# Optimization experiments

Measured on AMD Instinct MI355X. Metric: run time of the kernel, lower is better.

The kernel has to match this reference:

```python
import jax, jax.numpy as jnp
import numpy as np

# dims: StyleGAN2 modulated conv at 64x64, 512 channels
B, IC, OC, K, SD, H, W = 16, 512, 512, 3, 512, 64, 64
EPS = 1e-8


def setup_inputs() -> dict:
    key = jax.random.key(0)
    k1, k2, k3, k4 = jax.random.split(key, 4)
    return {
        "input": jax.random.normal(k1, (B, IC, H, W), dtype=jnp.float32),
        "style": jax.random.normal(k2, (B, SD), dtype=jnp.float32),
        # learned params
        "weight": jax.random.normal(k3, (1, OC, IC, K, K), dtype=jnp.float32),
        "mod_weight": jax.random.normal(k4, (IC, SD), dtype=jnp.float32),
        "mod_bias": jnp.ones((IC,), dtype=jnp.float32),  # bias_init=1
    }


def reference(input, style, weight, mod_weight, mod_bias):
    conv_scale = 1.0 / np.sqrt(IC * K * K)   # 1/sqrt(fan_in)
    mod_scale = 1.0 / np.sqrt(SD)            # EqualLinear scale, lr_mul=1

    # style modulation: EqualLinear(style_dim -> in_channel), no activation
    s = style @ (mod_weight * mod_scale).T + mod_bias          # [B, IC]

    # per-sample modulated weight [B, OC, IC, K, K]
    w = conv_scale * weight * s[:, None, :, None, None]
    # demodulation over (in_channel, kh, kw)
    demod = jax.lax.rsqrt(jnp.sum(w * w, axis=(2, 3, 4)) + EPS)  # [B, OC]
    w = w * demod[:, :, None, None, None]

    # grouped conv with groups=batch (same trick as torch F.conv2d groups=B)
    x = input.reshape(1, B * IC, H, W)
    wg = w.reshape(B * OC, IC, K, K)
    pad = K // 2
    out = jax.lax.conv_general_dilated(
        x, wg,
        window_strides=(1, 1),
        padding=[(pad, pad), (pad, pad)],
        dimension_numbers=("NCHW", "OIHW", "NCHW"),
        feature_group_count=B,
    )
    return out.reshape(B, OC, H, W)
```

## Files before the change

### kernel.cpp

```cpp
#include <hip/hip_runtime.h>
#include <hip/hip_bf16.h>

constexpr int BB = 16, IC = 512, OC = 512, HH = 64, WW = 64, HW = 64 * 64, SD = 512;
constexpr float MOD_SCALE = 0.04419417382415922f;
constexpr float CONV_SCALE = 0.014731391274719739f;
constexpr float CONV_SCALE2 = 2.170138888888889e-4f;

typedef float f32x4 __attribute__((ext_vector_type(4)));
typedef short bf16x8 __attribute__((ext_vector_type(8)));

__device__ __forceinline__ unsigned short f2bf(float x) {
  __hip_bfloat16 h = __float2bfloat16(x);
  return *(unsigned short*)&h;
}

__global__ void k_style(const float* __restrict__ style, const float* __restrict__ mw,
                        const float* __restrict__ mb, float* __restrict__ s) {
  __shared__ float st[SD];
  const int b = blockIdx.x;
  for (int i = threadIdx.x; i < SD; i += 256) st[i] = style[b * SD + i];
  __syncthreads();
  for (int ic = threadIdx.x; ic < IC; ic += 256) {
    const float4* wr = (const float4*)(mw + (size_t)ic * SD);
    float acc = 0.f;
    for (int d = 0; d < SD / 4; ++d) {
      float4 w4 = wr[d];
      float4 s4 = *(const float4*)&st[d * 4];
      acc += w4.x * s4.x + w4.y * s4.y + w4.z * s4.z + w4.w * s4.w;
    }
    s[b * IC + ic] = acc * MOD_SCALE + mb[ic];
  }
}

__global__ void k_pack(const float* __restrict__ w, unsigned short* __restrict__ wpack,
                       float* __restrict__ w2sum) {
  const int oc = blockIdx.x;
  const int ic0 = threadIdx.x * 2;
  const float* p = w + (size_t)oc * IC * 9 + (size_t)ic0 * 9;
  float v[18];
#pragma unroll
  for (int i = 0; i < 18; ++i) v[i] = p[i];
  float s0 = 0.f, s1 = 0.f;
#pragma unroll
  for (int t = 0; t < 9; ++t) { s0 += v[t] * v[t]; s1 += v[9 + t] * v[9 + t]; }
  *(float2*)&w2sum[oc * IC + ic0] = make_float2(s0, s1);
#pragma unroll
  for (int t = 0; t < 9; ++t) {
    unsigned int pk = (unsigned int)f2bf(v[t]) | ((unsigned int)f2bf(v[9 + t]) << 16);
    *(unsigned int*)&wpack[((size_t)t * OC + oc) * IC + ic0] = pk;
  }
}

__global__ void k_demod(const float* __restrict__ s, const float* __restrict__ w2sum,
                        float* __restrict__ fscale) {
  __shared__ float s2[IC];
  const int b = blockIdx.x;
  for (int i = threadIdx.x; i < IC; i += 256) { float v = s[b * IC + i]; s2[i] = v * v; }
  __syncthreads();
  for (int oc = threadIdx.x; oc < OC; oc += 256) {
    const float4* wr = (const float4*)(w2sum + (size_t)oc * IC);
    float acc = 0.f;
    for (int i4 = 0; i4 < IC / 4; ++i4) {
      float4 w4 = wr[i4];
      float4 q4 = *(const float4*)&s2[i4 * 4];
      acc += w4.x * q4.x + w4.y * q4.y + w4.z * q4.z + w4.w * q4.w;
    }
    fscale[b * OC + oc] = CONV_SCALE * rsqrtf(CONV_SCALE2 * acc + 1e-8f);
  }
}

__global__ __launch_bounds__(256) void k_conv(
    const float* __restrict__ x, const unsigned short* __restrict__ wpack,
    const float* __restrict__ s, const float* __restrict__ fscale,
    float* __restrict__ out) {
  __shared__ __align__(128) unsigned short Asm[3][128 * 32];
  __shared__ __align__(128) unsigned short Bsm[264 * 32];

  const int bx = blockIdx.x;
  const int b = bx >> 7;
  const int mblk = (bx >> 5) & 3;
  const int nblk = bx & 31;

  const int tid = threadIdx.x;
  const int wave = tid >> 6, lane = tid & 63;
  const int wm = wave >> 1, wn = wave & 1;
  const int lrow = lane & 15, lk = lane >> 4;

  const int h0 = nblk * 2;
  const float* xb = x + (size_t)b * IC * HW;
  const float* sb = s + b * IC;

  f32x4 acc[4][4];
#pragma unroll
  for (int i = 0; i < 4; ++i)
#pragma unroll
    for (int j = 0; j < 4; ++j) acc[i][j] = f32x4{0.f, 0.f, 0.f, 0.f};

  {
    int q = tid >> 5;
    int hh = q >> 1, wz = (q & 1) ? 65 : 0;
    Bsm[(hh * 66 + wz) * 32 + (tid & 31)] = 0;
  }

  auto stageB = [&](int icb) {
    const int hh = wave;
    const int w = lane;
    const int h_abs = h0 - 1 + hh;
    const bool vh = (h_abs >= 0) && (h_abs < HH);
    const int h_safe = vh ? h_abs : 0;
    const int r = hh * 66 + w + 1;
    const int swz = (r >> 1) & 3;
    const float* src = xb + (size_t)(icb * 32) * HW + h_safe * WW + w;
#pragma unroll
    for (int c = 0; c < 4; ++c) {
      unsigned int pk[4];
#pragma unroll
      for (int jj = 0; jj < 4; ++jj) {
        int ic = c * 8 + jj * 2;
        float m0 = vh ? sb[icb * 32 + ic] : 0.f;
        float m1 = vh ? sb[icb * 32 + ic + 1] : 0.f;
        float v0 = src[(size_t)ic * HW] * m0;
        float v1 = src[(size_t)(ic + 1) * HW] * m1;
        pk[jj] = (unsigned int)f2bf(v0) | ((unsigned int)f2bf(v1) << 16);
      }
      int cd = c ^ swz;
      *(uint4*)&Bsm[r * 32 + cd * 8] = make_uint4(pk[0], pk[1], pk[2], pk[3]);
    }
  };

  auto issueA = [&](int tap, int icb, int nb) {
    const unsigned short* base =
        wpack + ((size_t)(tap * OC + mblk * 128)) * IC + icb * 32;
#pragma unroll
    for (int q = 0; q < 2; ++q) {
      int r = wave * 32 + q * 16 + (lane >> 2);
      int c = lane & 3;
      int cs = c ^ ((r >> 1) & 3);
      const unsigned short* g = base + (size_t)r * IC + cs * 8;
      unsigned short* l = &Asm[nb][(wave * 32 + q * 16) * 32];
      __builtin_amdgcn_global_load_lds(
          (const __attribute__((address_space(1))) void*)g,
          (__attribute__((address_space(3))) void*)l, 16, 0, 0);
    }
  };

  stageB(0);
  issueA(0, 0, 0);
  issueA(1, 0, 1);
  __syncthreads();

  for (int icb = 0; icb < 16; ++icb) {
#pragma unroll
    for (int t = 0; t < 9; ++t) {
      if (t == 8) {
        if (icb == 15) asm volatile("s_waitcnt vmcnt(0)" ::: "memory");
        else           asm volatile("s_waitcnt vmcnt(2)" ::: "memory");
      } else {
        asm volatile("s_waitcnt vmcnt(2)" ::: "memory");
      }
      __builtin_amdgcn_s_barrier();
      __builtin_amdgcn_sched_barrier(0);

      if (t == 0 && icb > 0) {
        stageB(icb);
        asm volatile("s_waitcnt lgkmcnt(0)" ::: "memory");
        __builtin_amdgcn_s_barrier();
        __builtin_amdgcn_sched_barrier(0);
      }

      if (t <= 6) {
        issueA(t + 2, icb, (t + 2) % 3);
      } else if (icb < 15) {
        issueA(t - 7, icb + 1, t - 7);
      }

      bf16x8 af[4], bfr[4];
#pragma unroll
      for (int i = 0; i < 4; ++i) {
        int r = wm * 64 + i * 16 + lrow;
        af[i] = *(const bf16x8*)&Asm[t % 3][r * 32 + ((lk ^ ((r >> 1) & 3)) * 8)];
      }
      const int dh = t / 3 - 1, dw = t % 3 - 1;
      const int hb = wn + dh + 1;
#pragma unroll
      for (int j = 0; j < 4; ++j) {
        int r = hb * 66 + j * 16 + lrow + dw + 1;
        bfr[j] = *(const bf16x8*)&Bsm[r * 32 + ((lk ^ ((r >> 1) & 3)) * 8)];
      }
      __builtin_amdgcn_s_setprio(1);
#pragma unroll
      for (int i = 0; i < 4; ++i)
#pragma unroll
        for (int j = 0; j < 4; ++j)
          acc[i][j] =
              __builtin_amdgcn_mfma_f32_16x16x32_bf16(af[i], bfr[j], acc[i][j], 0, 0, 0);
      __builtin_amdgcn_s_setprio(0);
      __builtin_amdgcn_sched_barrier(0);
    }
  }

  const float* fsb = fscale + b * OC;
#pragma unroll
  for (int i = 0; i < 4; ++i) {
#pragma unroll
    for (int rr = 0; rr < 4; ++rr) {
      const int oc = mblk * 128 + wm * 64 + i * 16 + lk * 4 + rr;
      const float sc = fsb[oc];
      float* orow = out + ((size_t)(b * OC + oc)) * HW + nblk * 128 + wn * 64 + lrow;
#pragma unroll
      for (int j = 0; j < 4; ++j) orow[j * 16] = acc[i][j][rr] * sc;
    }
  }
}

extern "C" void kernel_launch(void* const* d_in, const int* in_sizes, int n_in,
                              void* d_out, int out_size, void* d_ws, size_t ws_size,
                              hipStream_t stream) {
  const float* input = (const float*)d_in[0];
  const float* style = (const float*)d_in[1];
  const float* weight = (const float*)d_in[2];
  const float* mod_weight = (const float*)d_in[3];
  const float* mod_bias = (const float*)d_in[4];
  float* out = (float*)d_out;

  char* ws = (char*)d_ws;
  constexpr size_t WPACK_B = (size_t)9 * OC * IC * 2;
  constexpr size_t W2SUM_B = (size_t)OC * IC * 4;
  constexpr size_t S_B = (size_t)BB * IC * 4;
  unsigned short* wpack = (unsigned short*)ws;
  float* w2sum = (float*)(ws + WPACK_B);
  float* s = (float*)(ws + WPACK_B + W2SUM_B);
  float* fscale = (float*)(ws + WPACK_B + W2SUM_B + S_B);

  k_style<<<BB, 256, 0, stream>>>(style, mod_weight, mod_bias, s);
  k_pack<<<OC, 256, 0, stream>>>(weight, wpack, w2sum);
  k_demod<<<BB, 256, 0, stream>>>(s, w2sum, fscale);
  k_conv<<<2048, 256, 0, stream>>>(input, wpack, s, fscale, out);
}
```

Baseline: 474.3 us.

## Deepen A-tile ring, drop per-tap barriers, prefetch input into registers

The A weight tiles now use a 4-deep LDS ring loaded three taps ahead. Each wave loads and reads only its own 32 rows, so the per-tap block-wide barriers are removed and only vmcnt waits remain. The next input-channel block of x is loaded into registers in the middle of the tap loop and written to LDS between blocks, which hides the global load latency of the B staging. The wave tiling changes from a 2x2 layout to a 4x1 layout (32 OC by 128 pixels per wave), and launch bounds request 3 blocks per CU. The cost is more registers for xv and more LDS, plus hand-tuned waitcnt counts that must match the exact load ordering.

```diff
diff --git a/kernel.cpp b/kernel.cpp
--- a/kernel.cpp
+++ b/kernel.cpp
@@ -8,6 +8,8 @@
 
 typedef float f32x4 __attribute__((ext_vector_type(4)));
 typedef short bf16x8 __attribute__((ext_vector_type(8)));
+
+#define VMWAIT(n) asm volatile("s_waitcnt vmcnt(" #n ")" ::: "memory")
 
 __device__ __forceinline__ unsigned short f2bf(float x) {
   __hip_bfloat16 h = __float2bfloat16(x);
@@ -69,32 +71,27 @@
   }
 }
 
-__global__ __launch_bounds__(256) void k_conv(
+__global__ __launch_bounds__(256, 3) void k_conv(
     const float* __restrict__ x, const unsigned short* __restrict__ wpack,
     const float* __restrict__ s, const float* __restrict__ fscale,
     float* __restrict__ out) {
-  __shared__ __align__(128) unsigned short Asm[3][128 * 32];
+  __shared__ __align__(128) unsigned short Asm[4][128 * 32];
   __shared__ __align__(128) unsigned short Bsm[264 * 32];
 
   const int bx = blockIdx.x;
-  const int b = bx >> 7;
-  const int mblk = (bx >> 5) & 3;
-  const int nblk = bx & 31;
-
+  const int b = bx >> 7, mblk = (bx >> 5) & 3, nblk = bx & 31;
   const int tid = threadIdx.x;
   const int wave = tid >> 6, lane = tid & 63;
-  const int wm = wave >> 1, wn = wave & 1;
   const int lrow = lane & 15, lk = lane >> 4;
-
   const int h0 = nblk * 2;
   const float* xb = x + (size_t)b * IC * HW;
   const float* sb = s + b * IC;
 
-  f32x4 acc[4][4];
-#pragma unroll
-  for (int i = 0; i < 4; ++i)
-#pragma unroll
-    for (int j = 0; j < 4; ++j) acc[i][j] = f32x4{0.f, 0.f, 0.f, 0.f};
+  f32x4 acc[2][8];
+#pragma unroll
+  for (int i = 0; i < 2; ++i)
+#pragma unroll
+    for (int j = 0; j < 8; ++j) acc[i][j] = f32x4{0.f, 0.f, 0.f, 0.f};
 
   {
     int q = tid >> 5;
@@ -102,40 +99,39 @@
     Bsm[(hh * 66 + wz) * 32 + (tid & 31)] = 0;
   }
 
-  auto stageB = [&](int icb) {
-    const int hh = wave;
-    const int w = lane;
-    const int h_abs = h0 - 1 + hh;
-    const bool vh = (h_abs >= 0) && (h_abs < HH);
-    const int h_safe = vh ? h_abs : 0;
-    const int r = hh * 66 + w + 1;
-    const int swz = (r >> 1) & 3;
-    const float* src = xb + (size_t)(icb * 32) * HW + h_safe * WW + w;
+  const int sh = h0 - 1 + wave;
+  const bool vh = (sh >= 0) && (sh < HH);
+  const int shs = vh ? sh : 0;
+  const int brow = wave * 66 + lane + 1;
+  const int bswz = (brow >> 1) & 3;
+
+  float xv[32];
+  auto ld_x = [&](int icb) {
+    const float* src = xb + (size_t)(icb * 32) * HW + shs * WW + lane;
+#pragma unroll
+    for (int k = 0; k < 32; ++k) xv[k] = src[(size_t)k * HW];
+  };
+  auto wr_B = [&](int icb) {
 #pragma unroll
     for (int c = 0; c < 4; ++c) {
       unsigned int pk[4];
 #pragma unroll
       for (int jj = 0; jj < 4; ++jj) {
-        int ic = c * 8 + jj * 2;
-        float m0 = vh ? sb[icb * 32 + ic] : 0.f;
-        float m1 = vh ? sb[icb * 32 + ic + 1] : 0.f;
-        float v0 = src[(size_t)ic * HW] * m0;
-        float v1 = src[(size_t)(ic + 1) * HW] * m1;
-        pk[jj] = (unsigned int)f2bf(v0) | ((unsigned int)f2bf(v1) << 16);
+        int k = c * 8 + jj * 2;
+        float m0 = vh ? sb[icb * 32 + k] : 0.f;
+        float m1 = vh ? sb[icb * 32 + k + 1] : 0.f;
+        pk[jj] = (unsigned int)f2bf(xv[k] * m0) | ((unsigned int)f2bf(xv[k + 1] * m1) << 16);
       }
-      int cd = c ^ swz;
-      *(uint4*)&Bsm[r * 32 + cd * 8] = make_uint4(pk[0], pk[1], pk[2], pk[3]);
-    }
-  };
-
+      *(uint4*)&Bsm[brow * 32 + ((c ^ bswz) * 8)] = make_uint4(pk[0], pk[1], pk[2], pk[3]);
+    }
+  };
   auto issueA = [&](int tap, int icb, int nb) {
     const unsigned short* base =
         wpack + ((size_t)(tap * OC + mblk * 128)) * IC + icb * 32;
 #pragma unroll
     for (int q = 0; q < 2; ++q) {
       int r = wave * 32 + q * 16 + (lane >> 2);
-      int c = lane & 3;
-      int cs = c ^ ((r >> 1) & 3);
+      int cs = (lane & 3) ^ ((r >> 1) & 3);
       const unsigned short* g = base + (size_t)r * IC + cs * 8;
       unsigned short* l = &Asm[nb][(wave * 32 + q * 16) * 32];
       __builtin_amdgcn_global_load_lds(
@@ -144,71 +140,83 @@
     }
   };
 
-  stageB(0);
+  auto do_tap = [&](int t, int bufr) {
+    bf16x8 af[2], bfr[8];
+#pragma unroll
+    for (int i = 0; i < 2; ++i) {
+      int r = wave * 32 + i * 16 + lrow;
+      af[i] = *(const bf16x8*)&Asm[bufr][r * 32 + ((lk ^ ((r >> 1) & 3)) * 8)];
+    }
+    const int dh = t / 3 - 1, dw = t % 3 - 1;
+#pragma unroll
+    for (int j = 0; j < 8; ++j) {
+      int r = ((j >> 2) + dh + 1) * 66 + (j & 3) * 16 + lrow + dw + 1;
+      bfr[j] = *(const bf16x8*)&Bsm[r * 32 + ((lk ^ ((r >> 1) & 3)) * 8)];
+    }
+    __builtin_amdgcn_s_setprio(1);
+#pragma unroll
+    for (int i = 0; i < 2; ++i)
+#pragma unroll
+      for (int j = 0; j < 8; ++j)
+        acc[i][j] =
+            __builtin_amdgcn_mfma_f32_16x16x32_bf16(af[i], bfr[j], acc[i][j], 0, 0, 0);
+    __builtin_amdgcn_s_setprio(0);
+  };
+
+  ld_x(0);
   issueA(0, 0, 0);
   issueA(1, 0, 1);
-  __syncthreads();
-
-  for (int icb = 0; icb < 16; ++icb) {
+  issueA(2, 0, 2);
+  wr_B(0);
+  asm volatile("s_waitcnt lgkmcnt(0)" ::: "memory");
+  __builtin_amdgcn_sched_barrier(0);
+  __builtin_amdgcn_s_barrier();
+
+  int pb = 0;
+  for (int icb = 0; icb < 15; ++icb) {
 #pragma unroll
     for (int t = 0; t < 9; ++t) {
-      if (t == 8) {
-        if (icb == 15) asm volatile("s_waitcnt vmcnt(0)" ::: "memory");
-        else           asm volatile("s_waitcnt vmcnt(2)" ::: "memory");
-      } else {
-        asm volatile("s_waitcnt vmcnt(2)" ::: "memory");
+      if (t < 6) VMWAIT(4); else VMWAIT(20);
+      if (t + 3 <= 8) issueA(t + 3, icb, (pb + t + 3) & 3);
+      else            issueA(t - 6, icb + 1, (pb + t + 3) & 3);
+      if (t == 5) ld_x(icb + 1);
+      do_tap(t, (pb + t) & 3);
+    }
+    __builtin_amdgcn_s_barrier();
+    __builtin_amdgcn_sched_barrier(0);
+    wr_B(icb + 1);
+    asm volatile("s_waitcnt lgkmcnt(0)" ::: "memory");
+    __builtin_amdgcn_sched_barrier(0);
+    __builtin_amdgcn_s_barrier();
+    pb += 9;
+  }
+#pragma unroll
+  for (int t = 0; t < 9; ++t) {
+    if (t < 6) {
+      VMWAIT(4);
+      issueA(t + 3, 15, (pb + t + 3) & 3);
+    } else if (t == 6) {
+      VMWAIT(4);
+    } else if (t == 7) {
+      VMWAIT(2);
+    } else {
+      VMWAIT(0);
+    }
+    do_tap(t, (pb + t) & 3);
+  }
+
+  const float* fsb = fscale + b * OC;
+#pragma unroll
+  for (int i = 0; i < 2; ++i) {
+#pragma unroll
+    for (int rr = 0; rr < 4; ++rr) {
+      const int oc = mblk * 128 + wave * 32 + i * 16 + lk * 4 + rr;
+      const float sc = fsb[oc];
+#pragma unroll
+      for (int j = 0; j < 8; ++j) {
+        out[((size_t)(b * OC + oc)) * HW + (h0 + (j >> 2)) * WW + (j & 3) * 16 + lrow] =
+            acc[i][j][rr] * sc;
       }
-      __builtin_amdgcn_s_barrier();
-      __builtin_amdgcn_sched_barrier(0);
-
-      if (t == 0 && icb > 0) {
-        stageB(icb);
-        asm volatile("s_waitcnt lgkmcnt(0)" ::: "memory");
-        __builtin_amdgcn_s_barrier();
-        __builtin_amdgcn_sched_barrier(0);
-      }
-
-      if (t <= 6) {
-        issueA(t + 2, icb, (t + 2) % 3);
-      } else if (icb < 15) {
-        issueA(t - 7, icb + 1, t - 7);
-      }
-
-      bf16x8 af[4], bfr[4];
-#pragma unroll
-      for (int i = 0; i < 4; ++i) {
-        int r = wm * 64 + i * 16 + lrow;
-        af[i] = *(const bf16x8*)&Asm[t % 3][r * 32 + ((lk ^ ((r >> 1) & 3)) * 8)];
-      }
-      const int dh = t / 3 - 1, dw = t % 3 - 1;
-      const int hb = wn + dh + 1;
-#pragma unroll
-      for (int j = 0; j < 4; ++j) {
-        int r = hb * 66 + j * 16 + lrow + dw + 1;
-        bfr[j] = *(const bf16x8*)&Bsm[r * 32 + ((lk ^ ((r >> 1) & 3)) * 8)];
-      }
-      __builtin_amdgcn_s_setprio(1);
-#pragma unroll
-      for (int i = 0; i < 4; ++i)
-#pragma unroll
-        for (int j = 0; j < 4; ++j)
-          acc[i][j] =
-              __builtin_amdgcn_mfma_f32_16x16x32_bf16(af[i], bfr[j], acc[i][j], 0, 0, 0);
-      __builtin_amdgcn_s_setprio(0);
-      __builtin_amdgcn_sched_barrier(0);
-    }
-  }
-
-  const float* fsb = fscale + b * OC;
-#pragma unroll
-  for (int i = 0; i < 4; ++i) {
-#pragma unroll
-    for (int rr = 0; rr < 4; ++rr) {
-      const int oc = mblk * 128 + wm * 64 + i * 16 + lk * 4 + rr;
-      const float sc = fsb[oc];
-      float* orow = out + ((size_t)(b * OC + oc)) * HW + nblk * 128 + wn * 64 + lrow;
-#pragma unroll
-      for (int j = 0; j < 4; ++j) orow[j * 16] = acc[i][j][rr] * sc;
     }
   }
 }
```

Measured after the change: 658.4 us. +38.8%, slower.

## Deepen A-tile prefetch to four LDS buffers and double-buffer B fragments

Applied to the files above, without the earlier changes.

Grows the weight-tile LDS ring from three to four buffers so async global-to-LDS loads run three taps ahead, relaxing the vmcnt waits. B fragments for the next tap are read from LDS between MFMA groups into a second register buffer, overlapping LDS reads with matrix math. Launch bounds now request three blocks per SIMD/CU, which caps registers and may force spills given the larger fragment state and extra LDS per block.

```diff
diff --git a/kernel.cpp b/kernel.cpp
--- a/kernel.cpp
+++ b/kernel.cpp
@@ -8,6 +8,8 @@
 
 typedef float f32x4 __attribute__((ext_vector_type(4)));
 typedef short bf16x8 __attribute__((ext_vector_type(8)));
+
+#define VMWAIT(n) asm volatile("s_waitcnt vmcnt(" #n ")" ::: "memory")
 
 __device__ __forceinline__ unsigned short f2bf(float x) {
   __hip_bfloat16 h = __float2bfloat16(x);
@@ -69,11 +71,11 @@
   }
 }
 
-__global__ __launch_bounds__(256) void k_conv(
+__global__ __launch_bounds__(256, 3) void k_conv(
     const float* __restrict__ x, const unsigned short* __restrict__ wpack,
     const float* __restrict__ s, const float* __restrict__ fscale,
     float* __restrict__ out) {
-  __shared__ __align__(128) unsigned short Asm[3][128 * 32];
+  __shared__ __align__(128) unsigned short Asm[4][128 * 32];
   __shared__ __align__(128) unsigned short Bsm[264 * 32];
 
   const int bx = blockIdx.x;
@@ -134,8 +136,7 @@
 #pragma unroll
     for (int q = 0; q < 2; ++q) {
       int r = wave * 32 + q * 16 + (lane >> 2);
-      int c = lane & 3;
-      int cs = c ^ ((r >> 1) & 3);
+      int cs = (lane & 3) ^ ((r >> 1) & 3);
       const unsigned short* g = base + (size_t)r * IC + cs * 8;
       unsigned short* l = &Asm[nb][(wave * 32 + q * 16) * 32];
       __builtin_amdgcn_global_load_lds(
@@ -144,56 +145,65 @@
     }
   };
 
+  auto loadB = [&](bf16x8* dst, int tn) {
+    const int dh = tn / 3 - 1, dw = tn % 3 - 1;
+    const int hb = wn + dh + 1;
+#pragma unroll
+    for (int j = 0; j < 4; ++j) {
+      int r = hb * 66 + j * 16 + lrow + dw + 1;
+      dst[j] = *(const bf16x8*)&Bsm[r * 32 + ((lk ^ ((r >> 1) & 3)) * 8)];
+    }
+  };
+
   stageB(0);
   issueA(0, 0, 0);
   issueA(1, 0, 1);
+  issueA(2, 0, 2);
   __syncthreads();
 
+  bf16x8 bfr[2][4];
+
   for (int icb = 0; icb < 16; ++icb) {
 #pragma unroll
     for (int t = 0; t < 9; ++t) {
-      if (t == 8) {
-        if (icb == 15) asm volatile("s_waitcnt vmcnt(0)" ::: "memory");
-        else           asm volatile("s_waitcnt vmcnt(2)" ::: "memory");
-      } else {
-        asm volatile("s_waitcnt vmcnt(2)" ::: "memory");
-      }
+      if (icb == 15 && t == 7)      { VMWAIT(2); }
+      else if (icb == 15 && t == 8) { VMWAIT(0); }
+      else                          { VMWAIT(4); }
       __builtin_amdgcn_s_barrier();
       __builtin_amdgcn_sched_barrier(0);
 
-      if (t == 0 && icb > 0) {
-        stageB(icb);
-        asm volatile("s_waitcnt lgkmcnt(0)" ::: "memory");
-        __builtin_amdgcn_s_barrier();
-        __builtin_amdgcn_sched_barrier(0);
+      if (t == 0) {
+        if (icb > 0) {
+          stageB(icb);
+          asm volatile("s_waitcnt lgkmcnt(0)" ::: "memory");
+          __builtin_amdgcn_s_barrier();
+          __builtin_amdgcn_sched_barrier(0);
+        }
+        loadB(bfr[0], 0);
       }
 
-      if (t <= 6) {
-        issueA(t + 2, icb, (t + 2) % 3);
-      } else if (icb < 15) {
-        issueA(t - 7, icb + 1, t - 7);
-      }
-
-      bf16x8 af[4], bfr[4];
+      if (t <= 5)          issueA(t + 3, icb, (icb + t + 3) & 3);
+      else if (icb < 15)   issueA(t - 6, icb + 1, (icb + t + 3) & 3);
+
+      bf16x8 af[4];
 #pragma unroll
       for (int i = 0; i < 4; ++i) {
         int r = wm * 64 + i * 16 + lrow;
-        af[i] = *(const bf16x8*)&Asm[t % 3][r * 32 + ((lk ^ ((r >> 1) & 3)) * 8)];
+        af[i] = *(const bf16x8*)&Asm[(icb + t) & 3][r * 32 + ((lk ^ ((r >> 1) & 3)) * 8)];
       }
-      const int dh = t / 3 - 1, dw = t % 3 - 1;
-      const int hb = wn + dh + 1;
-#pragma unroll
-      for (int j = 0; j < 4; ++j) {
-        int r = hb * 66 + j * 16 + lrow + dw + 1;
-        bfr[j] = *(const bf16x8*)&Bsm[r * 32 + ((lk ^ ((r >> 1) & 3)) * 8)];
-      }
+
       __builtin_amdgcn_s_setprio(1);
 #pragma unroll
-      for (int i = 0; i < 4; ++i)
+      for (int j = 0; j < 4; ++j)
+        acc[0][j] = __builtin_amdgcn_mfma_f32_16x16x32_bf16(af[0], bfr[t & 1][j],
+                                                            acc[0][j], 0, 0, 0);
+      if (t < 8) loadB(bfr[(t + 1) & 1], t + 1);
+#pragma unroll
+      for (int i = 1; i < 4; ++i)
 #pragma unroll
         for (int j = 0; j < 4; ++j)
-          acc[i][j] =
-              __builtin_amdgcn_mfma_f32_16x16x32_bf16(af[i], bfr[j], acc[i][j], 0, 0, 0);
+          acc[i][j] = __builtin_amdgcn_mfma_f32_16x16x32_bf16(af[i], bfr[t & 1][j],
+                                                              acc[i][j], 0, 0, 0);
       __builtin_amdgcn_s_setprio(0);
       __builtin_amdgcn_sched_barrier(0);
     }
```

After: 892.9 us. 88.3% more time.

## Give each wave private weight rows to drop per-tap barriers

Applied to the files above, without the earlier changes.

The wave tiling changes from 2x2 (64x64 per wave) to 4x1 (32 output channels x 128 pixels per wave). Each wave now reads only the weight-tile rows it loaded itself through global_load_lds, so the block-wide barrier before every tap can be dropped. Only the per-channel-block input restaging still needs barriers, and that restage moves to the end of each channel block. Each wave now issues more LDS reads for the input operand, and the kernel asks the compiler for three blocks per CU via launch bounds, which could add register pressure with the larger accumulator layout.

```diff
diff --git a/kernel.cpp b/kernel.cpp
--- a/kernel.cpp
+++ b/kernel.cpp
@@ -8,6 +8,8 @@
 
 typedef float f32x4 __attribute__((ext_vector_type(4)));
 typedef short bf16x8 __attribute__((ext_vector_type(8)));
+
+#define VMWAIT(n) asm volatile("s_waitcnt vmcnt(" #n ")" ::: "memory")
 
 __device__ __forceinline__ unsigned short f2bf(float x) {
   __hip_bfloat16 h = __float2bfloat16(x);
@@ -69,7 +71,7 @@
   }
 }
 
-__global__ __launch_bounds__(256) void k_conv(
+__global__ __launch_bounds__(256, 3) void k_conv(
     const float* __restrict__ x, const unsigned short* __restrict__ wpack,
     const float* __restrict__ s, const float* __restrict__ fscale,
     float* __restrict__ out) {
@@ -83,18 +85,17 @@
 
   const int tid = threadIdx.x;
   const int wave = tid >> 6, lane = tid & 63;
-  const int wm = wave >> 1, wn = wave & 1;
   const int lrow = lane & 15, lk = lane >> 4;
 
   const int h0 = nblk * 2;
   const float* xb = x + (size_t)b * IC * HW;
   const float* sb = s + b * IC;
 
-  f32x4 acc[4][4];
-#pragma unroll
-  for (int i = 0; i < 4; ++i)
-#pragma unroll
-    for (int j = 0; j < 4; ++j) acc[i][j] = f32x4{0.f, 0.f, 0.f, 0.f};
+  f32x4 acc[2][8];
+#pragma unroll
+  for (int i = 0; i < 2; ++i)
+#pragma unroll
+    for (int j = 0; j < 8; ++j) acc[i][j] = f32x4{0.f, 0.f, 0.f, 0.f};
 
   {
     int q = tid >> 5;
@@ -134,8 +135,7 @@
 #pragma unroll
     for (int q = 0; q < 2; ++q) {
       int r = wave * 32 + q * 16 + (lane >> 2);
-      int c = lane & 3;
-      int cs = c ^ ((r >> 1) & 3);
+      int cs = (lane & 3) ^ ((r >> 1) & 3);
       const unsigned short* g = base + (size_t)r * IC + cs * 8;
       unsigned short* l = &Asm[nb][(wave * 32 + q * 16) * 32];
       __builtin_amdgcn_global_load_lds(
@@ -152,21 +152,8 @@
   for (int icb = 0; icb < 16; ++icb) {
 #pragma unroll
     for (int t = 0; t < 9; ++t) {
-      if (t == 8) {
-        if (icb == 15) asm volatile("s_waitcnt vmcnt(0)" ::: "memory");
-        else           asm volatile("s_waitcnt vmcnt(2)" ::: "memory");
-      } else {
-        asm volatile("s_waitcnt vmcnt(2)" ::: "memory");
-      }
-      __builtin_amdgcn_s_barrier();
+      if (icb == 15 && t == 8) { VMWAIT(0); } else { VMWAIT(2); }
       __builtin_amdgcn_sched_barrier(0);
-
-      if (t == 0 && icb > 0) {
-        stageB(icb);
-        asm volatile("s_waitcnt lgkmcnt(0)" ::: "memory");
-        __builtin_amdgcn_s_barrier();
-        __builtin_amdgcn_sched_barrier(0);
-      }
 
       if (t <= 6) {
         issueA(t + 2, icb, (t + 2) % 3);
@@ -174,41 +161,54 @@
         issueA(t - 7, icb + 1, t - 7);
       }
 
-      bf16x8 af[4], bfr[4];
-#pragma unroll
-      for (int i = 0; i < 4; ++i) {
-        int r = wm * 64 + i * 16 + lrow;
-        af[i] = *(const bf16x8*)&Asm[t % 3][r * 32 + ((lk ^ ((r >> 1) & 3)) * 8)];
+      bf16x8 af0, af1;
+      {
+        int r0 = wave * 32 + lrow;
+        int r1 = wave * 32 + 16 + lrow;
+        af0 = *(const bf16x8*)&Asm[t % 3][r0 * 32 + ((lk ^ ((r0 >> 1) & 3)) * 8)];
+        af1 = *(const bf16x8*)&Asm[t % 3][r1 * 32 + ((lk ^ ((r1 >> 1) & 3)) * 8)];
       }
       const int dh = t / 3 - 1, dw = t % 3 - 1;
-      const int hb = wn + dh + 1;
-#pragma unroll
-      for (int j = 0; j < 4; ++j) {
-        int r = hb * 66 + j * 16 + lrow + dw + 1;
+      bf16x8 bfr[8];
+#pragma unroll
+      for (int j = 0; j < 8; ++j) {
+        int hb = (j >> 2) + dh + 1;
+        int r = hb * 66 + (j & 3) * 16 + lrow + dw + 1;
         bfr[j] = *(const bf16x8*)&Bsm[r * 32 + ((lk ^ ((r >> 1) & 3)) * 8)];
       }
+
       __builtin_amdgcn_s_setprio(1);
 #pragma unroll
-      for (int i = 0; i < 4; ++i)
-#pragma unroll
-        for (int j = 0; j < 4; ++j)
-          acc[i][j] =
-              __builtin_amdgcn_mfma_f32_16x16x32_bf16(af[i], bfr[j], acc[i][j], 0, 0, 0);
+      for (int j = 0; j < 8; ++j)
+        acc[0][j] = __builtin_amdgcn_mfma_f32_16x16x32_bf16(af0, bfr[j], acc[0][j], 0, 0, 0);
+#pragma unroll
+      for (int j = 0; j < 8; ++j)
+        acc[1][j] = __builtin_amdgcn_mfma_f32_16x16x32_bf16(af1, bfr[j], acc[1][j], 0, 0, 0);
       __builtin_amdgcn_s_setprio(0);
+    }
+
+    if (icb < 15) {
+      __builtin_amdgcn_s_barrier();
       __builtin_amdgcn_sched_barrier(0);
+      stageB(icb + 1);
+      asm volatile("s_waitcnt lgkmcnt(0)" ::: "memory");
+      __builtin_amdgcn_sched_barrier(0);
+      __builtin_amdgcn_s_barrier();
     }
   }
 
   const float* fsb = fscale + b * OC;
 #pragma unroll
-  for (int i = 0; i < 4; ++i) {
+  for (int i = 0; i < 2; ++i) {
 #pragma unroll
     for (int rr = 0; rr < 4; ++rr) {
-      const int oc = mblk * 128 + wm * 64 + i * 16 + lk * 4 + rr;
+      const int oc = mblk * 128 + wave * 32 + i * 16 + lk * 4 + rr;
       const float sc = fsb[oc];
-      float* orow = out + ((size_t)(b * OC + oc)) * HW + nblk * 128 + wn * 64 + lrow;
-#pragma unroll
-      for (int j = 0; j < 4; ++j) orow[j * 16] = acc[i][j][rr] * sc;
+      float* obase = out + ((size_t)(b * OC + oc)) * HW + nblk * 128;
+#pragma unroll
+      for (int j = 0; j < 8; ++j) {
+        obase[(j >> 2) * WW + (j & 3) * 16 + lrow] = acc[i][j][rr] * sc;
+      }
     }
   }
 }
```

After: 611.7 us. 29.0% more time.
